# Optimization experiments

Hardware: AMD Instinct MI355X
Metric: run time of the kernel (lower is better)

## Reference

```python
import jax, jax.numpy as jnp
import numpy as np

H = 256; NH = 4; DH = H // NH
NT, NS, NV = 4096, 2048, 1024
E1, E2, E3 = 65536, 16384, 32768
LN_EPS = 1e-5


def setup_inputs() -> dict:
    key = jax.random.key(0)
    ks = jax.random.split(key, 40)
    def nrm(i, shape):
        return jax.random.normal(ks[i], shape, jnp.float32) * 0.05
    inp = {
        "x_term": jax.random.normal(ks[0], (NT, H), jnp.float32),
        "x_symbol": jax.random.normal(ks[1], (NS, H), jnp.float32),
        "x_var": jax.random.normal(ks[2], (NV, H), jnp.float32),
        "ha_src": jax.random.randint(ks[3], (E1,), 0, NT),
        "ha_dst": jax.random.randint(ks[4], (E1,), 0, NT),
        "so_src": jax.random.randint(ks[5], (E2,), 0, NT),
        "so_dst": jax.random.randint(ks[6], (E2,), 0, NS),
        "vo_src": jax.random.randint(ks[7], (E3,), 0, NV),
        "vo_dst": jax.random.randint(ks[8], (E3,), 0, NT),
        # SAGEConv params for the 4 term-destination relations
        "Wl_rha": nrm(9, (H, H)),  "bl_rha": nrm(10, (H,)), "Wr_rha": nrm(11, (H, H)),
        "Wl_ha":  nrm(12, (H, H)), "bl_ha":  nrm(13, (H,)), "Wr_ha":  nrm(14, (H, H)),
        "Wl_rsym": nrm(15, (H, H)), "bl_rsym": nrm(16, (H,)), "Wr_rsym": nrm(17, (H, H)),
        "Wl_var": nrm(18, (H, H)), "bl_var": nrm(19, (H,)), "Wr_var": nrm(20, (H, H)),
        "ln_g": jnp.ones((H,), jnp.float32),
        "ln_b": jnp.zeros((H,), jnp.float32),
        "in_proj_w": nrm(21, (3 * H, H)),
        "in_proj_b": nrm(22, (3 * H,)),
        "out_proj_w": nrm(23, (H, H)),
        "out_proj_b": nrm(24, (H,)),
        "post_w": nrm(25, (H, H)),
        "post_b": nrm(26, (H,)),
    }
    return inp


def _sage(x_src, x_dst, src, dst, Wl, bl, Wr, num_dst):
    # PyG SAGEConv: lin_l(mean_j x_src[j]) + lin_r(x_dst)
    msg = x_src[src]                                            # [E, H] gather
    s = jax.ops.segment_sum(msg, dst, num_segments=num_dst)     # [N_dst, H] scatter-add
    cnt = jax.ops.segment_sum(jnp.ones((src.shape[0],), x_src.dtype), dst,
                              num_segments=num_dst)
    agg = s / jnp.maximum(cnt, 1.0)[:, None]
    return agg @ Wl.T + bl + x_dst @ Wr.T


def _layernorm(x, g, b):
    mu = jnp.mean(x, axis=-1, keepdims=True)
    var = jnp.mean(jnp.square(x - mu), axis=-1, keepdims=True)
    return (x - mu) * jax.lax.rsqrt(var + LN_EPS) * g + b


def _mha(x, in_w, in_b, out_w, out_b):
    # torch MultiheadAttention (eval, batch=1, self-attention)
    qkv = x @ in_w.T + in_b                       # [N, 3H]
    q, k, v = jnp.split(qkv, 3, axis=-1)
    def heads(t):
        return t.reshape(-1, NH, DH).transpose(1, 0, 2)  # [NH, N, DH]
    q, k, v = heads(q), heads(k), heads(v)
    scores = jnp.einsum("hqd,hkd->hqk", q, k) / np.sqrt(DH).astype(np.float32)
    a = jax.nn.softmax(scores, axis=-1)
    o = jnp.einsum("hqk,hkd->hqd", a, v)          # [NH, N, DH]
    o = o.transpose(1, 0, 2).reshape(-1, H)
    return o @ out_w.T + out_b


def reference(x_term, x_symbol, x_var,
              ha_src, ha_dst, so_src, so_dst, vo_src, vo_dst,
              Wl_rha, bl_rha, Wr_rha, Wl_ha, bl_ha, Wr_ha,
              Wl_rsym, bl_rsym, Wr_rsym, Wl_var, bl_var, Wr_var,
              ln_g, ln_b, in_proj_w, in_proj_b, out_proj_w, out_proj_b,
              post_w, post_b):
    nt = x_term.shape[0]
    # HeteroConv(aggr='sum') over the 4 relations whose destination is 'term'
    conv_term = (
        _sage(x_term, x_term, ha_dst, ha_src, Wl_rha, bl_rha, Wr_rha, nt)    # rev_has_arg
        + _sage(x_term, x_term, ha_src, ha_dst, Wl_ha, bl_ha, Wr_ha, nt)     # has_arg
        + _sage(x_symbol, x_term, so_dst, so_src, Wl_rsym, bl_rsym, Wr_rsym, nt)  # rev_symbol_of
        + _sage(x_var, x_term, vo_src, vo_dst, Wl_var, bl_var, Wr_var, nt)   # var_occurrence
    )
    term_out = _layernorm(conv_term + x_term, ln_g, ln_b)  # dropout is identity in eval
    attn_out = _mha(term_out, in_proj_w, in_proj_b, out_proj_w, out_proj_b)
    post = jax.nn.relu(attn_out @ post_w.T + post_b)
    term_final = post + term_out
    return term_final
```

## Files before the change

### kernel.cpp

```cpp
#include <hip/hip_runtime.h>
#include <hip/hip_bf16.h>

#define H 256
#define NT 4096
#define NHEAD 4
#define E1 65536
#define E2 16384
#define E3 32768
#define TOTE (2 * E1 + E2 + E3)
#define LN_EPS 1e-5f
#define SPLIT 4

typedef __hip_bfloat16 bf16;
typedef short bf16x8 __attribute__((ext_vector_type(8)));
typedef float f32x4 __attribute__((ext_vector_type(4)));

__device__ __forceinline__ float b2f(bf16 v) { return __bfloat162float(v); }
__device__ __forceinline__ float u2f(unsigned short u) {
    unsigned int x = ((unsigned int)u) << 16;
    return __uint_as_float(x);
}
__device__ __forceinline__ unsigned short f2u(float f) {
    bf16 h = __float2bfloat16(f);
    unsigned short v;
    __builtin_memcpy(&v, &h, 2);
    return v;
}
__device__ __forceinline__ unsigned short f2u_rtz(float f) {
    return (unsigned short)(__float_as_uint(f) >> 16);
}
__device__ __forceinline__ float ldin(const void* p, size_t i, bool isbf) {
    return isbf ? b2f(((const bf16*)p)[i]) : ((const float*)p)[i];
}

__global__ __launch_bounds__(256) void k_init(float4* cnt4, int n4,
                                              const unsigned int* __restrict__ lng,
                                              unsigned int* __restrict__ flag) {
    int i = blockIdx.x * 256 + threadIdx.x;
    if (i == 0) *flag = (lng[0] == 0x3F803F80u) ? 1u : 0u;
    int stride = gridDim.x * 256;
    float4 z = make_float4(0.f, 0.f, 0.f, 0.f);
    for (; i < n4; i += stride) cnt4[i] = z;
}

__global__ __launch_bounds__(256) void k_count4(const int* __restrict__ s0, const int* __restrict__ s1,
                                                const int* __restrict__ s2, const int* __restrict__ s3,
                                                int* __restrict__ cnt) {
    int i = blockIdx.x * 256 + threadIdx.x;
    int r, e;
    if (i < E1) { r = 0; e = i; }
    else if (i < 2 * E1) { r = 1; e = i - E1; }
    else if (i < 2 * E1 + E2) { r = 2; e = i - 2 * E1; }
    else if (i < TOTE) { r = 3; e = i - 2 * E1 - E2; }
    else return;
    const int* s = (r == 0) ? s0 : (r == 1) ? s1 : (r == 2) ? s2 : s3;
    atomicAdd(&cnt[r * NT + s[e]], 1);
}

__global__ __launch_bounds__(256) void k_scan(const int* __restrict__ cnt, int* __restrict__ offs,
                                              int* __restrict__ cursor) {
    __shared__ int tot[256];
    int t = threadIdx.x, r = blockIdx.x;
    const int* c = cnt + r * NT;
    int* o = offs + r * (NT + 1);
    int* cur = cursor + r * NT;
    int base = t * 16;
    int local[16];
    int sum = 0;
#pragma unroll
    for (int j = 0; j < 16; j++) { local[j] = c[base + j]; sum += local[j]; }
    tot[t] = sum;
    __syncthreads();
    if (t == 0) {
        int run = 0;
        for (int i = 0; i < 256; i++) { int v = tot[i]; tot[i] = run; run += v; }
        o[NT] = run;
    }
    __syncthreads();
    int run = tot[t];
#pragma unroll
    for (int j = 0; j < 16; j++) { o[base + j] = run; cur[base + j] = run; run += local[j]; }
}

__global__ __launch_bounds__(256) void k_fill(const int* __restrict__ s0, const int* __restrict__ s1,
                                              const int* __restrict__ s2, const int* __restrict__ s3,
                                              const int* __restrict__ g0, const int* __restrict__ g1,
                                              const int* __restrict__ g2, const int* __restrict__ g3,
                                              int* __restrict__ cursor, int* __restrict__ csr) {
    int i = blockIdx.x * 256 + threadIdx.x;
    int r, e, rb;
    if (i < E1) { r = 0; e = i; rb = 0; }
    else if (i < 2 * E1) { r = 1; e = i - E1; rb = E1; }
    else if (i < 2 * E1 + E2) { r = 2; e = i - 2 * E1; rb = 2 * E1; }
    else if (i < TOTE) { r = 3; e = i - 2 * E1 - E2; rb = 2 * E1 + E2; }
    else return;
    const int* s = (r == 0) ? s0 : (r == 1) ? s1 : (r == 2) ? s2 : s3;
    const int* g = (r == 0) ? g0 : (r == 1) ? g1 : (r == 2) ? g2 : g3;
    int d = s[e];
    int pos = atomicAdd(&cursor[r * NT + d], 1);
    csr[rb + pos] = g[e];
}

__global__ __launch_bounds__(256) void k_gatherA(
    const void* __restrict__ x0, const void* __restrict__ x1,
    const void* __restrict__ x2, const void* __restrict__ x3,
    const int* __restrict__ offs, const int* __restrict__ csr,
    bf16* __restrict__ aggs, const unsigned int* __restrict__ flag) {
    int y = blockIdx.y;
    int i = blockIdx.x * 4 + (threadIdx.x >> 6);
    int lane = threadIdx.x & 63;
    bool isbf = (*flag != 0u);
    const void* x = (y == 0) ? x0 : (y == 1) ? x1 : (y == 2) ? x2 : x3;
    static const int rbase[4] = {0, E1, 2 * E1, 2 * E1 + E2};
    const int* o = offs + y * (NT + 1);
    const int* cs = csr + rbase[y];
    int b = o[i], e = o[i + 1];
    float ax = 0.f, ay = 0.f, az = 0.f, aw = 0.f;
    if (isbf) {
        for (int j = b; j < e; j++) {
            int s = cs[j];
            ushort4 u = *(const ushort4*)((const unsigned short*)x + (size_t)s * H + lane * 4);
            ax += u2f(u.x); ay += u2f(u.y); az += u2f(u.z); aw += u2f(u.w);
        }
    } else {
        for (int j = b; j < e; j++) {
            int s = cs[j];
            float4 v = *(const float4*)((const float*)x + (size_t)s * H + lane * 4);
            ax += v.x; ay += v.y; az += v.z; aw += v.w;
        }
    }
    float inv = 1.0f / fmaxf((float)(e - b), 1.0f);
    *(ushort4*)((unsigned short*)aggs + ((size_t)y * NT + i) * H + lane * 4) =
        make_ushort4(f2u(ax * inv), f2u(ay * inv), f2u(az * inv), f2u(aw * inv));
}

__global__ __launch_bounds__(256) void k_prepB(
    const void* __restrict__ Wl0, const void* __restrict__ Wl1,
    const void* __restrict__ Wl2, const void* __restrict__ Wl3,
    const void* __restrict__ Wr0, const void* __restrict__ Wr1,
    const void* __restrict__ Wr2, const void* __restrict__ Wr3,
    const void* __restrict__ b0, const void* __restrict__ b1,
    const void* __restrict__ b2, const void* __restrict__ b3,
    bf16* __restrict__ Bcat, float* __restrict__ bsum, const unsigned int* __restrict__ flag) {
    int idx = blockIdx.x * 256 + threadIdx.x;
    bool isbf = (*flag != 0u);
    int n = idx / 1280, k = idx % 1280;
    float v;
    if (k < 1024) {
        const void* W = (k < 256) ? Wl0 : (k < 512) ? Wl1 : (k < 768) ? Wl2 : Wl3;
        v = ldin(W, (size_t)n * 256 + (k & 255), isbf);
    } else {
        size_t o = (size_t)n * 256 + (k - 1024);
        v = ldin(Wr0, o, isbf) + ldin(Wr1, o, isbf) + ldin(Wr2, o, isbf) + ldin(Wr3, o, isbf);
    }
    ((unsigned short*)Bcat)[idx] = f2u(v);
    if (idx < 256)
        bsum[idx] = ldin(b0, idx, isbf) + ldin(b1, idx, isbf) + ldin(b2, idx, isbf) + ldin(b3, idx, isbf);
}

__global__ __launch_bounds__(256) void k_convln(
    const bf16* __restrict__ aggs, const bf16* __restrict__ Bcat, const float* __restrict__ bsum,
    const void* __restrict__ xt, const void* __restrict__ gw, const void* __restrict__ gb,
    bf16* __restrict__ term, const unsigned int* __restrict__ flag) {
    __shared__ unsigned short Asm[8 * 16 * 8];
    __shared__ unsigned short Bsm[8 * 256 * 8];
    __shared__ float redS[4][16];
    const bool isbf = (*flag != 0u);
    const int tid = threadIdx.x;
    const int w = tid >> 6, lane = tid & 63;
    const int col = lane & 15, quad = lane >> 4;
    const int m0 = blockIdx.x * 16;
    const int srow = tid & 63, skq = tid >> 6;

    f32x4 acc[4];
#pragma unroll
    for (int dt = 0; dt < 4; dt++) acc[dt] = (f32x4){0.f, 0.f, 0.f, 0.f};

    bf16x8 areg;
    bf16x8 breg[8];
    auto loadA = [&](int k0) {
        if (tid < 128) {
            int row = tid & 15, akq = tid >> 4;
            int k = k0 + akq * 8;
            if (k < 1024) {
                areg = *(const bf16x8*)((const unsigned short*)aggs +
                                        ((size_t)(k >> 8) * NT + m0 + row) * 256 + (k & 255));
            } else {
#pragma unroll
                for (int j = 0; j < 8; j++)
                    areg[j] = (short)f2u(ldin(xt, (size_t)(m0 + row) * 256 + (k - 1024) + j, isbf));
            }
        }
    };
    auto loadB = [&](int k0) {
#pragma unroll
        for (int t = 0; t < 4; t++)
#pragma unroll
            for (int kk = 0; kk < 2; kk++)
                breg[t * 2 + kk] = *(const bf16x8*)((const unsigned short*)Bcat +
                                       (size_t)(t * 64 + srow) * 1280 + k0 + (skq * 2 + kk) * 8);
    };

    loadA(0);
    loadB(0);
    for (int k0 = 0; k0 < 1280; k0 += 64) {
        __syncthreads();
        if (tid < 128) *(bf16x8*)&Asm[tid * 8] = areg;
#pragma unroll
        for (int t = 0; t < 4; t++)
#pragma unroll
            for (int kk = 0; kk < 2; kk++)
                *(bf16x8*)&Bsm[((skq * 2 + kk) * 256 + t * 64 + srow) * 8] = breg[t * 2 + kk];
        __syncthreads();
        if (k0 + 64 < 1280) { loadA(k0 + 64); loadB(k0 + 64); }
#pragma unroll
        for (int ch = 0; ch < 2; ch++) {
            bf16x8 a = *(const bf16x8*)&Asm[(((ch * 4 + quad) & 7) * 16 + col) * 8];
#pragma unroll
            for (int dt = 0; dt < 4; dt++) {
                bf16x8 b = *(const bf16x8*)&Bsm[((ch * 4 + quad) * 256 + w * 64 + dt * 16 + col) * 8];
                acc[dt] = __builtin_amdgcn_mfma_f32_16x16x32_bf16(a, b, acc[dt], 0, 0, 0);
            }
        }
    }

#pragma unroll
    for (int dt = 0; dt < 4; dt++) {
        int n = w * 64 + dt * 16 + col;
        float bsv = bsum[n];
#pragma unroll
        for (int r = 0; r < 4; r++) {
            int m = m0 + quad * 4 + r;
            acc[dt][r] += bsv + ldin(xt, (size_t)m * 256 + n, isbf);
        }
    }
    float mu[4], rs_[4];
#pragma unroll
    for (int r = 0; r < 4; r++) {
        float s = acc[0][r] + acc[1][r] + acc[2][r] + acc[3][r];
#pragma unroll
        for (int mk = 1; mk <= 8; mk <<= 1) s += __shfl_xor(s, mk);
        if (col == 0) redS[w][quad * 4 + r] = s;
    }
    __syncthreads();
#pragma unroll
    for (int r = 0; r < 4; r++) {
        int m = quad * 4 + r;
        mu[r] = (redS[0][m] + redS[1][m] + redS[2][m] + redS[3][m]) * (1.0f / 256.0f);
    }
    __syncthreads();
#pragma unroll
    for (int r = 0; r < 4; r++) {
        float s2 = 0.f;
#pragma unroll
        for (int dt = 0; dt < 4; dt++) {
            float d = acc[dt][r] - mu[r];
            s2 += d * d;
        }
#pragma unroll
        for (int mk = 1; mk <= 8; mk <<= 1) s2 += __shfl_xor(s2, mk);
        if (col == 0) redS[w][quad * 4 + r] = s2;
    }
    __syncthreads();
#pragma unroll
    for (int r = 0; r < 4; r++) {
        int m = quad * 4 + r;
        float var = (redS[0][m] + redS[1][m] + redS[2][m] + redS[3][m]) * (1.0f / 256.0f);
        rs_[r] = rsqrtf(var + LN_EPS);
    }
#pragma unroll
    for (int dt = 0; dt < 4; dt++) {
        int n = w * 64 + dt * 16 + col;
        float gv = ldin(gw, n, isbf), bv = ldin(gb, n, isbf);
#pragma unroll
        for (int r = 0; r < 4; r++) {
            int m = m0 + quad * 4 + r;
            term[(size_t)m * 256 + n] = __float2bfloat16((acc[dt][r] - mu[r]) * rs_[r] * gv + bv);
        }
    }
}

template <int AMODE, int EPI>
__global__ __launch_bounds__(256) void k_gemm(
    const void* __restrict__ A, const void* __restrict__ A2, const float* __restrict__ ml,
    const void* __restrict__ B, const void* __restrict__ bias,
    const bf16* __restrict__ resid, bf16* __restrict__ vt, void* __restrict__ outp,
    int M, int N, int K, const unsigned int* __restrict__ flag) {
    __shared__ unsigned short Asm[4 * 64 * 8];
    __shared__ unsigned short Bsm[4 * 64 * 8];
    const bool isbf = (*flag != 0u);
    const int tid = threadIdx.x;
    const int w = tid >> 6, lane = tid & 63;
    const int col = lane & 15, quad = lane >> 4;
    const int m0 = blockIdx.x * 64, n0 = blockIdx.y * 64;
    const int srow = tid & 63, skq = tid >> 6;
    const int am = m0 + srow;

    f32x4 acc[4];
#pragma unroll
    for (int dt = 0; dt < 4; dt++) acc[dt] = (f32x4){0.f, 0.f, 0.f, 0.f};

    bf16x8 areg, breg;
    auto loadA = [&](int k0) {
        int k = k0 + skq * 8;
        if (AMODE == 0) {
            areg = *(const bf16x8*)((const unsigned short*)A + (size_t)am * K + k);
        } else {
            int h = k >> 6;
            float l0 = ml[(size_t)(0 * NHEAD + h) * NT + am];
            float l1 = ml[(size_t)(1 * NHEAD + h) * NT + am];
            float l2 = ml[(size_t)(2 * NHEAD + h) * NT + am];
            float l3 = ml[(size_t)(3 * NHEAD + h) * NT + am];
            float iw = 1.0f / (l0 + l1 + l2 + l3);
            bf16x8 o0 = *(const bf16x8*)((const unsigned short*)A + (size_t)am * H + k);
            bf16x8 o1 = *(const bf16x8*)((const unsigned short*)A + ((size_t)NT + am) * H + k);
            bf16x8 o2 = *(const bf16x8*)((const unsigned short*)A2 + (size_t)am * H + k);
            bf16x8 o3 = *(const bf16x8*)((const unsigned short*)A2 + ((size_t)NT + am) * H + k);
#pragma unroll
            for (int j = 0; j < 8; j++)
                areg[j] = (short)f2u((l0 * u2f((unsigned short)o0[j]) + l1 * u2f((unsigned short)o1[j]) +
                                      l2 * u2f((unsigned short)o2[j]) + l3 * u2f((unsigned short)o3[j])) * iw);
        }
    };
    auto loadB = [&](int k0) {
        size_t bi = (size_t)(n0 + srow) * K + k0 + skq * 8;
        if (isbf) {
            breg = *(const bf16x8*)((const unsigned short*)B + bi);
        } else {
#pragma unroll
            for (int j = 0; j < 8; j++) breg[j] = (short)f2u(((const float*)B)[bi + j]);
        }
    };

    loadA(0);
    loadB(0);
    for (int k0 = 0; k0 < K; k0 += 32) {
        __syncthreads();
        *(bf16x8*)&Asm[tid * 8] = areg;
        *(bf16x8*)&Bsm[tid * 8] = breg;
        __syncthreads();
        if (k0 + 32 < K) { loadA(k0 + 32); loadB(k0 + 32); }
        bf16x8 a = *(const bf16x8*)&Asm[(quad * 64 + w * 16 + col) * 8];
#pragma unroll
        for (int dt = 0; dt < 4; dt++) {
            bf16x8 b = *(const bf16x8*)&Bsm[(quad * 64 + dt * 16 + col) * 8];
            acc[dt] = __builtin_amdgcn_mfma_f32_16x16x32_bf16(a, b, acc[dt], 0, 0, 0);
        }
    }
#pragma unroll
    for (int dt = 0; dt < 4; dt++) {
        int n = n0 + dt * 16 + col;
        float bv = ldin(bias, n, isbf);
        if (EPI == 3 && n0 >= 512) {
            int m = m0 + w * 16 + quad * 4;
            *(ushort4*)((unsigned short*)vt + (size_t)(n - 512) * NT + m) =
                make_ushort4(f2u(acc[dt][0] + bv), f2u(acc[dt][1] + bv),
                             f2u(acc[dt][2] + bv), f2u(acc[dt][3] + bv));
            continue;
        }
#pragma unroll
        for (int r = 0; r < 4; r++) {
            int m = m0 + w * 16 + quad * 4 + r;
            float v = acc[dt][r] + bv;
            if (EPI == 3) {
                ((bf16*)outp)[(size_t)m * 512 + n] = __float2bfloat16(v);
            } else if (EPI == 2) {
                size_t off = (size_t)m * N + n;
                v = fmaxf(v, 0.f);
                v += b2f(resid[off]);
                ((float*)outp)[off] = v;
            } else {
                ((bf16*)outp)[(size_t)m * N + n] = __float2bfloat16(v);
            }
        }
    }
}

__global__ __launch_bounds__(256) void k_attn(const bf16* __restrict__ qkvQK,
                                              const bf16* __restrict__ vt,
                                              bf16* __restrict__ opart01,
                                              bf16* __restrict__ opart23,
                                              float* __restrict__ ml) {
    __shared__ unsigned short Ksm[8 * 64 * 8];
    __shared__ unsigned short Vsm[8 * 64 * 8];
    __shared__ unsigned short Psm[4][2048];
    const int h = blockIdx.y, sp = blockIdx.z;
    const int q0 = blockIdx.x * 128;
    const int tid = threadIdx.x;
    const int w = tid >> 6, lane = tid & 63;
    const int col = lane & 15, quad = lane >> 4;
    const unsigned short* qk = (const unsigned short*)qkvQK;
    const unsigned short* vp = (const unsigned short*)vt;

    bf16x8 aQ[2][2];
#pragma unroll
    for (int qt = 0; qt < 2; qt++)
#pragma unroll
        for (int ch = 0; ch < 2; ch++)
            aQ[qt][ch] = *(const bf16x8*)(qk + (size_t)(q0 + qt * 64 + w * 16 + col) * 512 +
                                          h * 64 + ch * 32 + quad * 8);

    f32x4 O[2][4];
#pragma unroll
    for (int qt = 0; qt < 2; qt++)
#pragma unroll
        for (int dt = 0; dt < 4; dt++) O[qt][dt] = (f32x4){0.f, 0.f, 0.f, 0.f};
    float lsum[2][4] = {};

    const int kbeg = sp * (NT / SPLIT), kend = kbeg + NT / SPLIT;
    const float SC = 0.125f * 1.44269504f;

    bf16x8 kreg[2], vreg[2];
    auto loadKV = [&](int kb) {
#pragma unroll
        for (int it = 0; it < 2; it++) {
            int cid = tid + it * 256;
            int kkey = cid & 63, dhq = cid >> 6;
            kreg[it] = *(const bf16x8*)(qk + (size_t)(kb + kkey) * 512 + 256 + h * 64 + dhq * 8);
            int vd = cid & 63, vo = cid >> 6;
            vreg[it] = *(const bf16x8*)(vp + (size_t)(h * 64 + vd) * NT + kb + vo * 8);
        }
    };
    loadKV(kbeg);

    for (int kb = kbeg; kb < kend; kb += 64) {
        __syncthreads();
#pragma unroll
        for (int it = 0; it < 2; it++) {
            int cid = tid + it * 256;
            *(bf16x8*)&Ksm[cid * 8] = kreg[it];
            *(bf16x8*)&Vsm[cid * 8] = vreg[it];
        }
        __syncthreads();
        if (kb + 64 < kend) loadKV(kb + 64);

        f32x4 c0[4], c1[4];
#pragma unroll
        for (int dt = 0; dt < 4; dt++) {
            c0[dt] = (f32x4){0.f, 0.f, 0.f, 0.f};
            c1[dt] = (f32x4){0.f, 0.f, 0.f, 0.f};
#pragma unroll
            for (int ch = 0; ch < 2; ch++) {
                bf16x8 b = *(const bf16x8*)&Ksm[((ch * 4 + quad) * 64 + dt * 16 + col) * 8];
                c0[dt] = __builtin_amdgcn_mfma_f32_16x16x32_bf16(aQ[0][ch], b, c0[dt], 0, 0, 0);
                c1[dt] = __builtin_amdgcn_mfma_f32_16x16x32_bf16(aQ[1][ch], b, c1[dt], 0, 0, 0);
            }
        }
#pragma unroll
        for (int qt = 0; qt < 2; qt++) {
#pragma unroll
            for (int dt = 0; dt < 4; dt++) {
                int k = dt * 16 + col;
#pragma unroll
                for (int r = 0; r < 4; r++) {
                    float p = exp2f((qt ? c1[dt][r] : c0[dt][r]) * SC);
                    lsum[qt][r] += p;
                    Psm[w][qt * 1024 + (k >> 3) * 128 + (quad * 4 + r) * 8 + (k & 7)] = f2u_rtz(p);
                }
            }
        }
        bf16x8 aP[2][2];
#pragma unroll
        for (int qt = 0; qt < 2; qt++)
#pragma unroll
            for (int kc = 0; kc < 2; kc++)
                aP[qt][kc] = *(const bf16x8*)&Psm[w][qt * 1024 + (kc * 4 + quad) * 128 + col * 8];
#pragma unroll
        for (int dt = 0; dt < 4; dt++)
#pragma unroll
            for (int kc = 0; kc < 2; kc++) {
                bf16x8 b = *(const bf16x8*)&Vsm[((kc * 4 + quad) * 64 + dt * 16 + col) * 8];
                O[0][dt] = __builtin_amdgcn_mfma_f32_16x16x32_bf16(aP[0][kc], b, O[0][dt], 0, 0, 0);
                O[1][dt] = __builtin_amdgcn_mfma_f32_16x16x32_bf16(aP[1][kc], b, O[1][dt], 0, 0, 0);
            }
    }
#pragma unroll
    for (int qt = 0; qt < 2; qt++) {
        float l[4];
#pragma unroll
        for (int r = 0; r < 4; r++) {
            float s = lsum[qt][r];
#pragma unroll
            for (int mk = 1; mk <= 8; mk <<= 1) s += __shfl_xor(s, mk);
            l[r] = s;
        }
        bf16* ob = (sp < 2) ? (opart01 + (size_t)sp * NT * H) : (opart23 + (size_t)(sp - 2) * NT * H);
#pragma unroll
        for (int dt = 0; dt < 4; dt++) {
#pragma unroll
            for (int r = 0; r < 4; r++) {
                int q = q0 + qt * 64 + w * 16 + quad * 4 + r;
                ob[(size_t)q * H + h * 64 + dt * 16 + col] = __float2bfloat16(O[qt][dt][r] / l[r]);
            }
        }
        if (col == 0) {
#pragma unroll
            for (int r = 0; r < 4; r++) {
                int q = q0 + qt * 64 + w * 16 + quad * 4 + r;
                ml[((size_t)sp * NHEAD + h) * NT + q] = l[r];
            }
        }
    }
}

extern "C" void kernel_launch(void* const* d_in, const int* in_sizes, int n_in,
                              void* d_out, int out_size, void* d_ws, size_t ws_size,
                              hipStream_t stream) {
    const void* x_term   = d_in[0];
    const void* x_symbol = d_in[1];
    const void* x_var    = d_in[2];
    const int* ha_src = (const int*)d_in[3];
    const int* ha_dst = (const int*)d_in[4];
    const int* so_src = (const int*)d_in[5];
    const int* so_dst = (const int*)d_in[6];
    const int* vo_src = (const int*)d_in[7];
    const int* vo_dst = (const int*)d_in[8];
    const void* Wl[4]  = {d_in[9],  d_in[12], d_in[15], d_in[18]};
    const void* blv[4] = {d_in[10], d_in[13], d_in[16], d_in[19]};
    const void* Wr[4]  = {d_in[11], d_in[14], d_in[17], d_in[20]};
    const void* ln_g = d_in[21];
    const void* ln_b = d_in[22];
    const void* in_w = d_in[23];
    const void* in_b = d_in[24];
    const void* out_w = d_in[25];
    const void* out_b = d_in[26];
    const void* post_w = d_in[27];
    const void* post_b = d_in[28];

    char* ws = (char*)d_ws;
    unsigned int* flag = (unsigned int*)ws;
    char* csrbase = ws + 256;
    int* cnt    = (int*)csrbase;
    int* offs   = (int*)(csrbase + 65536);
    int* cursor = (int*)(csrbase + 132096);
    int* csr    = (int*)(csrbase + 197632);
    bf16*  Bcat = (bf16*)csrbase;
    float* bsum = (float*)(csrbase + 655360);
    float* ml   = (float*)csrbase;
    bf16* aggs  = (bf16*)(ws + (1 << 20));
    bf16* term  = (bf16*)(ws + (1 << 20) + 8388608);
    bf16* opart23 = (bf16*)(ws + (1 << 20) + 10485760);
    bf16* qkvQK = aggs;
    bf16* vt    = (bf16*)((char*)aggs + 4194304);
    bf16* proj  = aggs;
    bf16* opart01 = (bf16*)d_out;

    k_init<<<16, 256, 0, stream>>>((float4*)cnt, 4 * NT / 4, (const unsigned int*)ln_g, flag);
    k_count4<<<(TOTE + 255) / 256, 256, 0, stream>>>(ha_src, ha_dst, so_src, vo_dst, cnt);
    k_scan<<<4, 256, 0, stream>>>(cnt, offs, cursor);
    k_fill<<<(TOTE + 255) / 256, 256, 0, stream>>>(ha_src, ha_dst, so_src, vo_dst,
                                                   ha_dst, ha_src, so_dst, vo_src, cursor, csr);
    k_gatherA<<<dim3(NT / 4, 4), 256, 0, stream>>>(x_term, x_term, x_symbol, x_var,
                                                   offs, csr, aggs, flag);
    k_prepB<<<(256 * 1280) / 256, 256, 0, stream>>>(Wl[0], Wl[1], Wl[2], Wl[3],
                                                    Wr[0], Wr[1], Wr[2], Wr[3],
                                                    blv[0], blv[1], blv[2], blv[3],
                                                    Bcat, bsum, flag);

    k_convln<<<256, 256, 0, stream>>>(aggs, Bcat, bsum, x_term, ln_g, ln_b, term, flag);

    k_gemm<0, 3><<<dim3(64, 12), 256, 0, stream>>>(
        term, nullptr, nullptr, in_w, in_b, nullptr, vt, qkvQK, NT, 768, 256, flag);

    k_attn<<<dim3(32, NHEAD, SPLIT), 256, 0, stream>>>(qkvQK, vt, opart01, opart23, ml);

    k_gemm<1, 0><<<dim3(64, 4), 256, 0, stream>>>(
        opart01, opart23, ml, out_w, out_b, nullptr, nullptr, proj, NT, 256, 256, flag);

    k_gemm<0, 2><<<dim3(64, 4), 256, 0, stream>>>(
        proj, nullptr, nullptr, post_w, post_b, term, nullptr, d_out, NT, 256, 256, flag);

    (void)in_sizes; (void)n_in; (void)out_size; (void)ws_size;
}
```

Measured before the change: 278.7 us.

## Deepen GEMM K-step to 64 and transpose QK^T MFMA for vectorized P stores

The generic GEMM now stages a 64-wide K slice per iteration, two 8-element chunks per thread, which halves the number of barrier pairs and doubles the MFMA work between syncs. The attention kernel swaps the MFMA operands so each lane holds four consecutive keys for one query. That lets P be written to shared memory as one ushort4 store instead of four scalar stores, and the row sum is reduced with two shuffles plus a broadcast. The cost is more registers and LDS in the GEMM, and the new P layout indexing must stay correct.

```diff
diff --git a/kernel.cpp b/kernel.cpp
--- a/kernel.cpp
+++ b/kernel.cpp
@@ -286,8 +286,8 @@
     const void* __restrict__ B, const void* __restrict__ bias,
     const bf16* __restrict__ resid, bf16* __restrict__ vt, void* __restrict__ outp,
     int M, int N, int K, const unsigned int* __restrict__ flag) {
-    __shared__ unsigned short Asm[4 * 64 * 8];
-    __shared__ unsigned short Bsm[4 * 64 * 8];
+    __shared__ unsigned short Asm[8 * 64 * 8];
+    __shared__ unsigned short Bsm[8 * 64 * 8];
     const bool isbf = (*flag != 0u);
     const int tid = threadIdx.x;
     const int w = tid >> 6, lane = tid & 63;
@@ -300,51 +300,63 @@
 #pragma unroll
     for (int dt = 0; dt < 4; dt++) acc[dt] = (f32x4){0.f, 0.f, 0.f, 0.f};
 
-    bf16x8 areg, breg;
+    bf16x8 areg[2], breg[2];
     auto loadA = [&](int k0) {
-        int k = k0 + skq * 8;
-        if (AMODE == 0) {
-            areg = *(const bf16x8*)((const unsigned short*)A + (size_t)am * K + k);
-        } else {
-            int h = k >> 6;
-            float l0 = ml[(size_t)(0 * NHEAD + h) * NT + am];
-            float l1 = ml[(size_t)(1 * NHEAD + h) * NT + am];
-            float l2 = ml[(size_t)(2 * NHEAD + h) * NT + am];
-            float l3 = ml[(size_t)(3 * NHEAD + h) * NT + am];
-            float iw = 1.0f / (l0 + l1 + l2 + l3);
-            bf16x8 o0 = *(const bf16x8*)((const unsigned short*)A + (size_t)am * H + k);
-            bf16x8 o1 = *(const bf16x8*)((const unsigned short*)A + ((size_t)NT + am) * H + k);
-            bf16x8 o2 = *(const bf16x8*)((const unsigned short*)A2 + (size_t)am * H + k);
-            bf16x8 o3 = *(const bf16x8*)((const unsigned short*)A2 + ((size_t)NT + am) * H + k);
-#pragma unroll
-            for (int j = 0; j < 8; j++)
-                areg[j] = (short)f2u((l0 * u2f((unsigned short)o0[j]) + l1 * u2f((unsigned short)o1[j]) +
-                                      l2 * u2f((unsigned short)o2[j]) + l3 * u2f((unsigned short)o3[j])) * iw);
+#pragma unroll
+        for (int c = 0; c < 2; c++) {
+            int k = k0 + skq * 16 + c * 8;
+            if (AMODE == 0) {
+                areg[c] = *(const bf16x8*)((const unsigned short*)A + (size_t)am * K + k);
+            } else {
+                int h = k >> 6;
+                float l0 = ml[(size_t)(0 * NHEAD + h) * NT + am];
+                float l1 = ml[(size_t)(1 * NHEAD + h) * NT + am];
+                float l2 = ml[(size_t)(2 * NHEAD + h) * NT + am];
+                float l3 = ml[(size_t)(3 * NHEAD + h) * NT + am];
+                float iw = 1.0f / (l0 + l1 + l2 + l3);
+                bf16x8 o0 = *(const bf16x8*)((const unsigned short*)A + (size_t)am * H + k);
+                bf16x8 o1 = *(const bf16x8*)((const unsigned short*)A + ((size_t)NT + am) * H + k);
+                bf16x8 o2 = *(const bf16x8*)((const unsigned short*)A2 + (size_t)am * H + k);
+                bf16x8 o3 = *(const bf16x8*)((const unsigned short*)A2 + ((size_t)NT + am) * H + k);
+#pragma unroll
+                for (int j = 0; j < 8; j++)
+                    areg[c][j] = (short)f2u((l0 * u2f((unsigned short)o0[j]) + l1 * u2f((unsigned short)o1[j]) +
+                                             l2 * u2f((unsigned short)o2[j]) + l3 * u2f((unsigned short)o3[j])) * iw);
+            }
         }
     };
     auto loadB = [&](int k0) {
-        size_t bi = (size_t)(n0 + srow) * K + k0 + skq * 8;
-        if (isbf) {
-            breg = *(const bf16x8*)((const unsigned short*)B + bi);
-        } else {
-#pragma unroll
-            for (int j = 0; j < 8; j++) breg[j] = (short)f2u(((const float*)B)[bi + j]);
+#pragma unroll
+        for (int c = 0; c < 2; c++) {
+            size_t bi = (size_t)(n0 + srow) * K + k0 + skq * 16 + c * 8;
+            if (isbf) {
+                breg[c] = *(const bf16x8*)((const unsigned short*)B + bi);
+            } else {
+#pragma unroll
+                for (int j = 0; j < 8; j++) breg[c][j] = (short)f2u(((const float*)B)[bi + j]);
+            }
         }
     };
 
     loadA(0);
     loadB(0);
-    for (int k0 = 0; k0 < K; k0 += 32) {
+    for (int k0 = 0; k0 < K; k0 += 64) {
         __syncthreads();
-        *(bf16x8*)&Asm[tid * 8] = areg;
-        *(bf16x8*)&Bsm[tid * 8] = breg;
+#pragma unroll
+        for (int c = 0; c < 2; c++) {
+            *(bf16x8*)&Asm[((skq * 2 + c) * 64 + srow) * 8] = areg[c];
+            *(bf16x8*)&Bsm[((skq * 2 + c) * 64 + srow) * 8] = breg[c];
+        }
         __syncthreads();
-        if (k0 + 32 < K) { loadA(k0 + 32); loadB(k0 + 32); }
-        bf16x8 a = *(const bf16x8*)&Asm[(quad * 64 + w * 16 + col) * 8];
-#pragma unroll
-        for (int dt = 0; dt < 4; dt++) {
-            bf16x8 b = *(const bf16x8*)&Bsm[(quad * 64 + dt * 16 + col) * 8];
-            acc[dt] = __builtin_amdgcn_mfma_f32_16x16x32_bf16(a, b, acc[dt], 0, 0, 0);
+        if (k0 + 64 < K) { loadA(k0 + 64); loadB(k0 + 64); }
+#pragma unroll
+        for (int ch = 0; ch < 2; ch++) {
+            bf16x8 a = *(const bf16x8*)&Asm[((ch * 4 + quad) * 64 + w * 16 + col) * 8];
+#pragma unroll
+            for (int dt = 0; dt < 4; dt++) {
+                bf16x8 b = *(const bf16x8*)&Bsm[((ch * 4 + quad) * 64 + dt * 16 + col) * 8];
+                acc[dt] = __builtin_amdgcn_mfma_f32_16x16x32_bf16(a, b, acc[dt], 0, 0, 0);
+            }
         }
     }
 #pragma unroll
@@ -405,10 +417,11 @@
     for (int qt = 0; qt < 2; qt++)
 #pragma unroll
         for (int dt = 0; dt < 4; dt++) O[qt][dt] = (f32x4){0.f, 0.f, 0.f, 0.f};
-    float lsum[2][4] = {};
+    float lsum[2] = {0.f, 0.f};
 
     const int kbeg = sp * (NT / SPLIT), kend = kbeg + NT / SPLIT;
     const float SC = 0.125f * 1.44269504f;
+    const int pbase = col * 8 + (quad & 1) * 4 + (quad >> 1) * 128;
 
     bf16x8 kreg[2], vreg[2];
     auto loadKV = [&](int kb) {
@@ -441,22 +454,21 @@
             c1[dt] = (f32x4){0.f, 0.f, 0.f, 0.f};
 #pragma unroll
             for (int ch = 0; ch < 2; ch++) {
-                bf16x8 b = *(const bf16x8*)&Ksm[((ch * 4 + quad) * 64 + dt * 16 + col) * 8];
-                c0[dt] = __builtin_amdgcn_mfma_f32_16x16x32_bf16(aQ[0][ch], b, c0[dt], 0, 0, 0);
-                c1[dt] = __builtin_amdgcn_mfma_f32_16x16x32_bf16(aQ[1][ch], b, c1[dt], 0, 0, 0);
+                bf16x8 kf = *(const bf16x8*)&Ksm[((ch * 4 + quad) * 64 + dt * 16 + col) * 8];
+                c0[dt] = __builtin_amdgcn_mfma_f32_16x16x32_bf16(kf, aQ[0][ch], c0[dt], 0, 0, 0);
+                c1[dt] = __builtin_amdgcn_mfma_f32_16x16x32_bf16(kf, aQ[1][ch], c1[dt], 0, 0, 0);
             }
         }
 #pragma unroll
         for (int qt = 0; qt < 2; qt++) {
 #pragma unroll
             for (int dt = 0; dt < 4; dt++) {
-                int k = dt * 16 + col;
-#pragma unroll
-                for (int r = 0; r < 4; r++) {
-                    float p = exp2f((qt ? c1[dt][r] : c0[dt][r]) * SC);
-                    lsum[qt][r] += p;
-                    Psm[w][qt * 1024 + (k >> 3) * 128 + (quad * 4 + r) * 8 + (k & 7)] = f2u_rtz(p);
-                }
+                f32x4 cc = qt ? c1[dt] : c0[dt];
+                float p0 = exp2f(cc[0] * SC), p1 = exp2f(cc[1] * SC);
+                float p2 = exp2f(cc[2] * SC), p3 = exp2f(cc[3] * SC);
+                lsum[qt] += (p0 + p1) + (p2 + p3);
+                *(ushort4*)&Psm[w][qt * 1024 + dt * 256 + pbase] =
+                    make_ushort4(f2u_rtz(p0), f2u_rtz(p1), f2u_rtz(p2), f2u_rtz(p3));
             }
         }
         bf16x8 aP[2][2];
@@ -476,28 +488,21 @@
     }
 #pragma unroll
     for (int qt = 0; qt < 2; qt++) {
-        float l[4];
-#pragma unroll
-        for (int r = 0; r < 4; r++) {
-            float s = lsum[qt][r];
-#pragma unroll
-            for (int mk = 1; mk <= 8; mk <<= 1) s += __shfl_xor(s, mk);
-            l[r] = s;
-        }
+        float l = lsum[qt];
+        l += __shfl_xor(l, 16);
+        l += __shfl_xor(l, 32);
         bf16* ob = (sp < 2) ? (opart01 + (size_t)sp * NT * H) : (opart23 + (size_t)(sp - 2) * NT * H);
+        if (quad == 0)
+            ml[((size_t)sp * NHEAD + h) * NT + (q0 + qt * 64 + w * 16 + col)] = l;
+        float lr[4];
+#pragma unroll
+        for (int r = 0; r < 4; r++) lr[r] = __shfl(l, quad * 4 + r, 16);
 #pragma unroll
         for (int dt = 0; dt < 4; dt++) {
 #pragma unroll
             for (int r = 0; r < 4; r++) {
                 int q = q0 + qt * 64 + w * 16 + quad * 4 + r;
-                ob[(size_t)q * H + h * 64 + dt * 16 + col] = __float2bfloat16(O[qt][dt][r] / l[r]);
-            }
-        }
-        if (col == 0) {
-#pragma unroll
-            for (int r = 0; r < 4; r++) {
-                int q = q0 + qt * 64 + w * 16 + quad * 4 + r;
-                ml[((size_t)sp * NHEAD + h) * NT + q] = l[r];
+                ob[(size_t)q * H + h * 64 + dt * 16 + col] = __float2bfloat16(O[qt][dt][r] / lr[r]);
             }
         }
     }
```

New measurement: 277.3 us. No clear change (-0.5%).
